# Kernel tuning notes

Measured on AMD Instinct MI355X. Metric: run time of the kernel, lower is better.

## Reference

```python
import jax, jax.numpy as jnp
import numpy as np

N = 50000      # nodes
E = 800000     # edges
F_IN = 128     # num_node_features
H = 128        # hidden_channels
C = 10         # num_classes
G = 512        # graphs in batch


def setup_inputs() -> dict:
    key = jax.random.key(0)
    ks = jax.random.split(key, 8)
    x = jax.random.normal(ks[0], (N, F_IN), dtype=jnp.float32)
    edge_index = jax.random.randint(ks[1], (2, E), 0, N, dtype=jnp.int64)
    batch = jnp.sort(jax.random.randint(ks[2], (N,), 0, G, dtype=jnp.int64))
    s = 1.0 / np.sqrt(F_IN)
    W1 = jax.random.normal(ks[3], (F_IN, H), dtype=jnp.float32) * s
    b1 = jnp.zeros((H,), dtype=jnp.float32)
    W2 = jax.random.normal(ks[4], (H, H), dtype=jnp.float32) * s
    b2 = jnp.zeros((H,), dtype=jnp.float32)
    Wl = jax.random.normal(ks[5], (H, C), dtype=jnp.float32) * s
    bl = jnp.zeros((C,), dtype=jnp.float32)
    return {"x": x, "edge_index": edge_index, "batch": batch,
            "W1": W1, "b1": b1, "W2": W2, "b2": b2, "Wl": Wl, "bl": bl}


def _gcn_conv(h, src, dst, deg_inv_sqrt, W, b):
    # PyG GCNConv: x @ W, then symmetric-normalized scatter-add with self-loops.
    h = h @ W                                   # [N, H]
    norm = deg_inv_sqrt[src] * deg_inv_sqrt[dst]  # [E]
    msg = h[src] * norm[:, None]                # gather + scale, [E, H]
    out = jax.ops.segment_sum(msg, dst, num_segments=N)
    # self-loop contribution (deg already includes +1):
    out = out + h * (deg_inv_sqrt * deg_inv_sqrt)[:, None]
    return out + b


def reference(x, edge_index, batch, W1, b1, W2, b2, Wl, bl):
    src, dst = edge_index[0], edge_index[1]
    # degree on destination nodes, +1 for self-loops (PyG default)
    deg = jax.ops.segment_sum(jnp.ones((E,), x.dtype), dst, num_segments=N) + 1.0
    deg_inv_sqrt = jax.lax.rsqrt(deg)

    h = jax.nn.relu(_gcn_conv(x, src, dst, deg_inv_sqrt, W1, b1))
    h = jax.nn.relu(_gcn_conv(h, src, dst, deg_inv_sqrt, W2, b2))

    # global mean pool over graphs
    sums = jax.ops.segment_sum(h, batch, num_segments=G)          # [G, H]
    counts = jax.ops.segment_sum(jnp.ones((N,), h.dtype), batch, num_segments=G)
    pooled = sums / jnp.clip(counts, 1.0)[:, None]
    # dropout p=0.5 is identity in eval mode
    return pooled @ Wl + bl
```

## Files before the change

### kernel.cpp

```cpp
#include <hip/hip_runtime.h>
#include <hip/hip_bf16.h>
#include <hip/hip_fp16.h>

typedef unsigned short ushort_t;
typedef unsigned int uint32;
typedef __attribute__((ext_vector_type(8))) _Float16 half8;
typedef __attribute__((ext_vector_type(4))) float floatx4;

#define KMAX 64
#define BSHIFT 6
#define BCAP2 1280
#define MAXBUK 800

__device__ __forceinline__ uint32 pack2h(float a, float b) {
    return (uint32)__half_as_ushort(__float2half(a)) |
           ((uint32)__half_as_ushort(__float2half(b)) << 16);
}
__device__ __forceinline__ float2 unpack2h(uint32 q) {
    __half2 hh = *reinterpret_cast<__half2*>(&q);
    return __half22float2(hh);
}

__global__ __launch_bounds__(256) void binmm_k(
    const int* __restrict__ ei, int* __restrict__ bcur,
    uint32* __restrict__ binned, int E, int nbuk, int BB,
    const float* __restrict__ x, const float* __restrict__ W,
    uint32* __restrict__ t2, int N,
    const int* __restrict__ batch, int* __restrict__ gstart, int G) {
    __shared__ __align__(16) char smem[34816];
    int tid = threadIdx.x;
    if (blockIdx.x < BB) {
        int* hist = (int*)smem;
        int* lbase = hist + MAXBUK;
        for (int i = tid; i < nbuk; i += 256) hist[i] = 0;
        __syncthreads();
        int base = blockIdx.x * 4096;
        uint32 ed[16];
        int bk[16];
        #pragma unroll
        for (int i = 0; i < 16; ++i) {
            int e = base + i * 256 + tid;
            if (e < E) {
                int s = ei[e], d = ei[E + e];
                ed[i] = (uint32)s | ((uint32)d << 16);
                bk[i] = d >> BSHIFT;
                atomicAdd(&hist[bk[i]], 1);
            } else bk[i] = -1;
        }
        __syncthreads();
        for (int i = tid; i < nbuk; i += 256) lbase[i] = atomicAdd(&bcur[i], hist[i]);
        __syncthreads();
        for (int i = tid; i < nbuk; i += 256) hist[i] = 0;
        __syncthreads();
        #pragma unroll
        for (int i = 0; i < 16; ++i) {
            if (bk[i] >= 0) {
                int p = atomicAdd(&hist[bk[i]], 1);
                int idx = lbase[bk[i]] + p;
                if (idx < BCAP2) binned[(size_t)bk[i] * BCAP2 + idx] = ed[i];
            }
        }
    } else {
        int bid = blockIdx.x - BB;
        int i0 = bid * 256 + tid;
        if (i0 <= G) {
            int lo = 0, hi = N;
            while (lo < hi) {
                int mid = (lo + hi) >> 1;
                if (batch[mid] < i0) lo = mid + 1; else hi = mid;
            }
            gstart[i0] = lo;
        }
        ushort_t (*Wh)[136] = (ushort_t(*)[136])smem;
        for (int i = tid; i < 128 * 128; i += 256) {
            int k = i >> 7, c = i & 127;
            Wh[c][k] = __half_as_ushort(__float2half(W[i]));
        }
        __syncthreads();

        int wave = tid >> 6, lane = tid & 63;
        int row0 = bid * 64 + wave * 16;
        int m = lane & 15;
        int arow = row0 + m;
        int koff = (lane >> 4) * 8;
        bool valid = arow < N;

        floatx4 acc[8];
        #pragma unroll
        for (int nt = 0; nt < 8; ++nt) acc[nt] = (floatx4){0.f, 0.f, 0.f, 0.f};

        for (int kk = 0; kk < 4; ++kk) {
            int k = kk * 32 + koff;
            union { uint32 u[4]; half8 h; } av;
            av.u[0] = av.u[1] = av.u[2] = av.u[3] = 0;
            if (valid) {
                const float* p = x + (size_t)arow * 128 + k;
                floatx4 f0 = *(const floatx4*)p;
                floatx4 f1 = *(const floatx4*)(p + 4);
                av.u[0] = pack2h(f0[0], f0[1]);
                av.u[1] = pack2h(f0[2], f0[3]);
                av.u[2] = pack2h(f1[0], f1[1]);
                av.u[3] = pack2h(f1[2], f1[3]);
            }
            half8 af = av.h;
            #pragma unroll
            for (int nt = 0; nt < 8; ++nt) {
                int col = nt * 16 + m;
                half8 bf = *(const half8*)(&Wh[col][k]);
                acc[nt] = __builtin_amdgcn_mfma_f32_16x16x32_f16(af, bf, acc[nt], 0, 0, 0);
            }
        }
        int r0 = (lane >> 4) * 4;
        #pragma unroll
        for (int nt = 0; nt < 4; ++nt) {
            int c = nt * 16 + m;
            #pragma unroll
            for (int r = 0; r < 4; ++r) {
                int row = row0 + r0 + r;
                if (row < N)
                    t2[(size_t)row * 64 + c] = pack2h(acc[nt][r], acc[nt + 4][r]);
            }
        }
    }
}

__global__ __launch_bounds__(256) void fill4_k(const uint32* __restrict__ binned,
                                               const int* __restrict__ bcur,
                                               int* __restrict__ cnt,
                                               ushort_t* __restrict__ slot,
                                               uint32* __restrict__ t2, int N) {
    __shared__ uint32 ls[64 * KMAX / 2];
    __shared__ int lc[64];
    __shared__ float dsf[64];
    int b = blockIdx.x;
    int tid = threadIdx.x;
    if (tid < 64) lc[tid] = 0;
    uint32 sv2 = (uint32)(ushort_t)N | ((uint32)(ushort_t)N << 16);
    for (int i = tid; i < 64 * KMAX / 2; i += 256) ls[i] = sv2;
    __syncthreads();
    int ne = bcur[b];
    if (ne > BCAP2) ne = BCAP2;
    const uint32* src = binned + (size_t)b * BCAP2;
    int nbase = b << BSHIFT;
    ushort_t* lsu = (ushort_t*)ls;
    for (int i = tid; i < ne; i += 256) {
        uint32 ed = src[i];
        int s = (int)(ed & 0xFFFFu);
        int d = (int)(ed >> 16) - nbase;
        int p = atomicAdd(&lc[d], 1);
        if (p < KMAX) lsu[(d << 6) + p] = (ushort_t)s;
    }
    __syncthreads();
    int nn = N - nbase;
    if (nn > 64) nn = 64;
    if (tid < 64) {
        if (tid < nn) cnt[nbase + tid] = lc[tid];
        dsf[tid] = rsqrtf((float)lc[tid] + 1.0f);
    }
    uint4* gs = (uint4*)(slot + ((size_t)nbase << 6));
    const uint4* lsv = (const uint4*)ls;
    int totalv = nn * 8;
    for (int i = tid; i < totalv; i += 256) gs[i] = lsv[i];
    __syncthreads();
    int tot = nn * 64;
    for (int i = tid; i < tot; i += 256) {
        int r = i >> 6, c = i & 63;
        size_t idx = ((size_t)(nbase + r) << 6) + c;
        float ds = dsf[r];
        float2 f = unpack2h(t2[idx]);
        t2[idx] = pack2h(f.x * ds, f.y * ds);
    }
}

__device__ __forceinline__ void gather16(const uint32* __restrict__ t2,
                                         const ushort_t* __restrict__ sl,
                                         int lane, float& acc0, float& acc1) {
    uint4 qa = *(const uint4*)(sl);
    uint4 qb = *(const uint4*)(sl + 8);
    uint32 sw[8] = {qa.x, qa.y, qa.z, qa.w, qb.x, qb.y, qb.z, qb.w};
    int s[16];
    #pragma unroll
    for (int u = 0; u < 8; ++u) {
        s[2 * u] = (int)(sw[u] & 0xFFFFu);
        s[2 * u + 1] = (int)(sw[u] >> 16);
    }
    float2 f[16];
    #pragma unroll
    for (int u = 0; u < 16; ++u)
        f[u] = unpack2h(t2[(size_t)s[u] * 64 + lane]);
    #pragma unroll
    for (int u = 0; u < 16; ++u) {
        acc0 += f[u].x;
        acc1 += f[u].y;
    }
}

__global__ __launch_bounds__(256) void agg_k(const uint32* __restrict__ t2,
                                             const int* __restrict__ cnt,
                                             const ushort_t* __restrict__ slot,
                                             const float* __restrict__ bias,
                                             uint32* __restrict__ outp, int N) {
    int wave = threadIdx.x >> 6, lane = threadIdx.x & 63;
    int n = blockIdx.x * 4 + wave;
    if (n >= N) return;
    int deg = cnt[n];
    float d = rsqrtf((float)deg + 1.0f);
    if (deg > KMAX) deg = KMAX;
    float2 self = unpack2h(t2[(size_t)n * 64 + lane]);
    float acc0 = self.x;
    float acc1 = self.y;
    const ushort_t* sl = slot + (size_t)n * KMAX;
    int rounds = (deg + 15) >> 4;
    for (int rr = 0; rr < rounds; ++rr)
        gather16(t2, sl + rr * 16, lane, acc0, acc1);
    acc0 = fmaxf(acc0 * d + bias[lane], 0.f);
    acc1 = fmaxf(acc1 * d + bias[lane + 64], 0.f);
    outp[(size_t)n * 64 + lane] = pack2h(acc0, acc1);
}

__global__ __launch_bounds__(256) void gemm2_k(const uint32* __restrict__ Av,
                                               const float* __restrict__ W,
                                               uint32* __restrict__ t2, int N,
                                               const int* __restrict__ cnt) {
    int tid = threadIdx.x;
    __shared__ ushort_t Wh[128][136];
    for (int i = tid; i < 128 * 128; i += 256) {
        int k = i >> 7, c = i & 127;
        Wh[c][k] = __half_as_ushort(__float2half(W[i]));
    }
    __syncthreads();

    int wave = tid >> 6, lane = tid & 63;
    int row0 = blockIdx.x * 64 + wave * 16;
    int m = lane & 15;
    int arow = row0 + m;
    int koff = (lane >> 4) * 8;
    bool valid = arow < N;

    floatx4 acc[8];
    #pragma unroll
    for (int nt = 0; nt < 8; ++nt) acc[nt] = (floatx4){0.f, 0.f, 0.f, 0.f};

    for (int kk = 0; kk < 4; ++kk) {
        int k = kk * 32 + koff;
        union { uint32 u[4]; half8 h; } av;
        av.u[0] = av.u[1] = av.u[2] = av.u[3] = 0;
        if (valid) {
            const uint32* hp = Av + (size_t)arow * 64 + (k & 63);
            uint4 w0 = *(const uint4*)hp;
            uint4 w1 = *(const uint4*)(hp + 4);
            uint32 ws[8] = {w0.x, w0.y, w0.z, w0.w, w1.x, w1.y, w1.z, w1.w};
            if (k >= 64) {
                #pragma unroll
                for (int j = 0; j < 4; ++j)
                    av.u[j] = (ws[2 * j] >> 16) | (ws[2 * j + 1] & 0xFFFF0000u);
            } else {
                #pragma unroll
                for (int j = 0; j < 4; ++j)
                    av.u[j] = (ws[2 * j] & 0xFFFFu) | (ws[2 * j + 1] << 16);
            }
        }
        half8 af = av.h;
        #pragma unroll
        for (int nt = 0; nt < 8; ++nt) {
            int col = nt * 16 + m;
            half8 bf = *(const half8*)(&Wh[col][k]);
            acc[nt] = __builtin_amdgcn_mfma_f32_16x16x32_f16(af, bf, acc[nt], 0, 0, 0);
        }
    }

    int r0 = (lane >> 4) * 4;
    float dsc[4];
    #pragma unroll
    for (int r = 0; r < 4; ++r) {
        int row = row0 + r0 + r;
        dsc[r] = (row < N) ? rsqrtf((float)cnt[row] + 1.0f) : 0.f;
    }
    #pragma unroll
    for (int nt = 0; nt < 4; ++nt) {
        int c = nt * 16 + m;
        #pragma unroll
        for (int r = 0; r < 4; ++r) {
            int row = row0 + r0 + r;
            if (row < N)
                t2[(size_t)row * 64 + c] =
                    pack2h(acc[nt][r] * dsc[r], acc[nt + 4][r] * dsc[r]);
        }
    }
}

__global__ __launch_bounds__(256) void aggpool_k(const uint32* __restrict__ t2,
                                                 const int* __restrict__ cnt,
                                                 const ushort_t* __restrict__ slot,
                                                 const float* __restrict__ bias,
                                                 const int* __restrict__ batch,
                                                 float* __restrict__ gsum, int N) {
    int wave = threadIdx.x >> 6, lane = threadIdx.x & 63;
    int n = blockIdx.x * 4 + wave;
    if (n >= N) return;
    int deg = cnt[n];
    float d = rsqrtf((float)deg + 1.0f);
    if (deg > KMAX) deg = KMAX;
    float2 self = unpack2h(t2[(size_t)n * 64 + lane]);
    float acc0 = self.x;
    float acc1 = self.y;
    const ushort_t* sl = slot + (size_t)n * KMAX;
    int rounds = (deg + 15) >> 4;
    for (int rr = 0; rr < rounds; ++rr)
        gather16(t2, sl + rr * 16, lane, acc0, acc1);
    acc0 = fmaxf(acc0 * d + bias[lane], 0.f);
    acc1 = fmaxf(acc1 * d + bias[lane + 64], 0.f);
    int g = batch[n];
    atomicAdd(&gsum[(size_t)g * 128 + lane], acc0);
    atomicAdd(&gsum[(size_t)g * 128 + 64 + lane], acc1);
}

__global__ __launch_bounds__(128) void poolfin_k(const float* __restrict__ gsum,
                                                 const int* __restrict__ gstart,
                                                 const float* __restrict__ Wl,
                                                 const float* __restrict__ bl,
                                                 float* __restrict__ out, int C) {
    __shared__ float m[128];
    int g = blockIdx.x;
    float inv = 1.f / fmaxf((float)(gstart[g + 1] - gstart[g]), 1.f);
    m[threadIdx.x] = gsum[(size_t)g * 128 + threadIdx.x] * inv;
    __syncthreads();
    if (threadIdx.x < C) {
        float sum = bl[threadIdx.x];
        #pragma unroll 4
        for (int jj = 0; jj < 128; ++jj)
            sum += m[jj] * Wl[jj * C + threadIdx.x];
        out[g * C + threadIdx.x] = sum;
    }
}

extern "C" void kernel_launch(void* const* d_in, const int* in_sizes, int n_in,
                              void* d_out, int out_size, void* d_ws, size_t ws_size,
                              hipStream_t stream) {
    const float* x   = (const float*)d_in[0];
    const int* ei    = (const int*)d_in[1];
    const int* batch = (const int*)d_in[2];
    const float* W1  = (const float*)d_in[3];
    const float* b1  = (const float*)d_in[4];
    const float* W2  = (const float*)d_in[5];
    const float* b2  = (const float*)d_in[6];
    const float* Wl  = (const float*)d_in[7];
    const float* bl  = (const float*)d_in[8];
    float* out = (float*)d_out;

    int N = in_sizes[2];
    int E = in_sizes[1] / 2;
    int C = in_sizes[8];
    int G = out_size / C;
    int nbuk = (N + 63) >> BSHIFT;

    char* w = (char*)d_ws;
    auto alloc = [&](size_t bytes) -> void* {
        void* p = (void*)w;
        w += (bytes + 255) & ~(size_t)255;
        return p;
    };
    int* bcur       = (int*)alloc((size_t)nbuk * 4);
    int* cnt        = (int*)alloc((size_t)N * 4);
    int* gstart     = (int*)alloc((size_t)(G + 1) * 4);
    ushort_t* slot  = (ushort_t*)alloc((size_t)nbuk * 64 * KMAX * 2);
    uint32* binned  = (uint32*)alloc((size_t)nbuk * BCAP2 * 4);
    uint32* t2      = (uint32*)alloc((size_t)(N + 1) * 64 * 4);
    uint32* h1      = (uint32*)alloc((size_t)N * 64 * 4);
    uint32* t2b     = (uint32*)alloc((size_t)(N + 1) * 64 * 4);
    float* gsum     = (float*)alloc((size_t)G * 128 * 4);

    hipMemsetAsync(bcur, 0, (size_t)nbuk * 4, stream);
    hipMemsetAsync(gsum, 0, (size_t)G * 128 * 4, stream);
    hipMemsetAsync(t2 + (size_t)N * 64, 0, 256, stream);
    hipMemsetAsync(t2b + (size_t)N * 64, 0, 256, stream);

    int GB = (N + 63) / 64;
    int AB = (N + 3) / 4;
    int BB = (E + 4095) / 4096;

    binmm_k<<<BB + GB, 256, 0, stream>>>(ei, bcur, binned, E, nbuk, BB,
                                         x, W1, t2, N, batch, gstart, G);
    fill4_k<<<nbuk, 256, 0, stream>>>(binned, bcur, cnt, slot, t2, N);
    agg_k<<<AB, 256, 0, stream>>>(t2, cnt, slot, b1, h1, N);
    gemm2_k<<<GB, 256, 0, stream>>>(h1, W2, t2b, N, cnt);
    aggpool_k<<<AB, 256, 0, stream>>>(t2b, cnt, slot, b2, batch, gsum, N);
    poolfin_k<<<G, 128, 0, stream>>>(gsum, gstart, Wl, bl, out, C);
}
```

Baseline: 202.0 us.

## Replace bucketed edge binning with direct global-atomic slot fill and drop fill kernel

Removes the two-phase bucket sort (shared histogram plus binned buffer) and the fill4_k kernel. Edges are now placed straight into per-node slot lists with global atomics on cnt, and the padding is a 0xFF sentinel set by a memset. Source-side degree scaling moves into the aggregation gather, which reads cnt for each neighbour and applies rsqrt there. Memsets for gsum and the sentinel rows are folded into the first kernel. In exchange there are heavily contended random global atomics, an extra memset of the slot array (about 6.4 MB), and an extra cnt load plus rsqrt per gathered neighbour. gemm2_k and aggpool_k are not shown changing, so if the scaling is not moved there too, layer-2 results may be wrong.

```diff
diff --git a/kernel.cpp b/kernel.cpp
--- a/kernel.cpp
+++ b/kernel.cpp
@@ -8,9 +8,7 @@
 typedef __attribute__((ext_vector_type(4))) float floatx4;
 
 #define KMAX 64
-#define BSHIFT 6
-#define BCAP2 1280
-#define MAXBUK 800
+#define SENT 65535
 
 __device__ __forceinline__ uint32 pack2h(float a, float b) {
     return (uint32)__half_as_ushort(__float2half(a)) |
@@ -22,43 +20,28 @@
 }
 
 __global__ __launch_bounds__(256) void binmm_k(
-    const int* __restrict__ ei, int* __restrict__ bcur,
-    uint32* __restrict__ binned, int E, int nbuk, int BB,
+    const int* __restrict__ ei, int* __restrict__ cnt,
+    ushort_t* __restrict__ slot, int E, int BB,
     const float* __restrict__ x, const float* __restrict__ W,
-    uint32* __restrict__ t2, int N,
+    uint32* __restrict__ t2, uint32* __restrict__ t2b,
+    float* __restrict__ gsum, int GS, int N,
     const int* __restrict__ batch, int* __restrict__ gstart, int G) {
-    __shared__ __align__(16) char smem[34816];
     int tid = threadIdx.x;
     if (blockIdx.x < BB) {
-        int* hist = (int*)smem;
-        int* lbase = hist + MAXBUK;
-        for (int i = tid; i < nbuk; i += 256) hist[i] = 0;
-        __syncthreads();
         int base = blockIdx.x * 4096;
-        uint32 ed[16];
-        int bk[16];
         #pragma unroll
         for (int i = 0; i < 16; ++i) {
             int e = base + i * 256 + tid;
             if (e < E) {
                 int s = ei[e], d = ei[E + e];
-                ed[i] = (uint32)s | ((uint32)d << 16);
-                bk[i] = d >> BSHIFT;
-                atomicAdd(&hist[bk[i]], 1);
-            } else bk[i] = -1;
-        }
-        __syncthreads();
-        for (int i = tid; i < nbuk; i += 256) lbase[i] = atomicAdd(&bcur[i], hist[i]);
-        __syncthreads();
-        for (int i = tid; i < nbuk; i += 256) hist[i] = 0;
-        __syncthreads();
-        #pragma unroll
-        for (int i = 0; i < 16; ++i) {
-            if (bk[i] >= 0) {
-                int p = atomicAdd(&hist[bk[i]], 1);
-                int idx = lbase[bk[i]] + p;
-                if (idx < BCAP2) binned[(size_t)bk[i] * BCAP2 + idx] = ed[i];
-            }
+                int p = atomicAdd(&cnt[d], 1);
+                if (p < KMAX) slot[(size_t)d * KMAX + p] = (ushort_t)s;
+            }
+        }
+        for (int i = blockIdx.x * 256 + tid; i < GS; i += BB * 256) gsum[i] = 0.f;
+        if (blockIdx.x == 0 && tid < 64) {
+            t2[(size_t)SENT * 64 + tid] = 0u;
+            t2b[(size_t)SENT * 64 + tid] = 0u;
         }
     } else {
         int bid = blockIdx.x - BB;
@@ -71,7 +54,7 @@
             }
             gstart[i0] = lo;
         }
-        ushort_t (*Wh)[136] = (ushort_t(*)[136])smem;
+        __shared__ ushort_t Wh[128][136];
         for (int i = tid; i < 128 * 128; i += 256) {
             int k = i >> 7, c = i & 127;
             Wh[c][k] = __half_as_ushort(__float2half(W[i]));
@@ -124,51 +107,30 @@
     }
 }
 
-__global__ __launch_bounds__(256) void fill4_k(const uint32* __restrict__ binned,
-                                               const int* __restrict__ bcur,
-                                               int* __restrict__ cnt,
-                                               ushort_t* __restrict__ slot,
-                                               uint32* __restrict__ t2, int N) {
-    __shared__ uint32 ls[64 * KMAX / 2];
-    __shared__ int lc[64];
-    __shared__ float dsf[64];
-    int b = blockIdx.x;
-    int tid = threadIdx.x;
-    if (tid < 64) lc[tid] = 0;
-    uint32 sv2 = (uint32)(ushort_t)N | ((uint32)(ushort_t)N << 16);
-    for (int i = tid; i < 64 * KMAX / 2; i += 256) ls[i] = sv2;
-    __syncthreads();
-    int ne = bcur[b];
-    if (ne > BCAP2) ne = BCAP2;
-    const uint32* src = binned + (size_t)b * BCAP2;
-    int nbase = b << BSHIFT;
-    ushort_t* lsu = (ushort_t*)ls;
-    for (int i = tid; i < ne; i += 256) {
-        uint32 ed = src[i];
-        int s = (int)(ed & 0xFFFFu);
-        int d = (int)(ed >> 16) - nbase;
-        int p = atomicAdd(&lc[d], 1);
-        if (p < KMAX) lsu[(d << 6) + p] = (ushort_t)s;
-    }
-    __syncthreads();
-    int nn = N - nbase;
-    if (nn > 64) nn = 64;
-    if (tid < 64) {
-        if (tid < nn) cnt[nbase + tid] = lc[tid];
-        dsf[tid] = rsqrtf((float)lc[tid] + 1.0f);
-    }
-    uint4* gs = (uint4*)(slot + ((size_t)nbase << 6));
-    const uint4* lsv = (const uint4*)ls;
-    int totalv = nn * 8;
-    for (int i = tid; i < totalv; i += 256) gs[i] = lsv[i];
-    __syncthreads();
-    int tot = nn * 64;
-    for (int i = tid; i < tot; i += 256) {
-        int r = i >> 6, c = i & 63;
-        size_t idx = ((size_t)(nbase + r) << 6) + c;
-        float ds = dsf[r];
-        float2 f = unpack2h(t2[idx]);
-        t2[idx] = pack2h(f.x * ds, f.y * ds);
+__device__ __forceinline__ void gather16s(const uint32* __restrict__ t2,
+                                          const int* __restrict__ cnt,
+                                          const ushort_t* __restrict__ sl,
+                                          int lane, float& acc0, float& acc1) {
+    uint4 qa = *(const uint4*)(sl);
+    uint4 qb = *(const uint4*)(sl + 8);
+    uint32 sw[8] = {qa.x, qa.y, qa.z, qa.w, qb.x, qb.y, qb.z, qb.w};
+    int s[16];
+    #pragma unroll
+    for (int u = 0; u < 8; ++u) {
+        s[2 * u] = (int)(sw[u] & 0xFFFFu);
+        s[2 * u + 1] = (int)(sw[u] >> 16);
+    }
+    float2 f[16];
+    float ds[16];
+    #pragma unroll
+    for (int u = 0; u < 16; ++u) {
+        f[u] = unpack2h(t2[(size_t)s[u] * 64 + lane]);
+        ds[u] = rsqrtf((float)cnt[s[u]] + 1.0f);
+    }
+    #pragma unroll
+    for (int u = 0; u < 16; ++u) {
+        acc0 = fmaf(f[u].x, ds[u], acc0);
+        acc1 = fmaf(f[u].y, ds[u], acc1);
     }
 }
 
@@ -207,12 +169,12 @@
     float d = rsqrtf((float)deg + 1.0f);
     if (deg > KMAX) deg = KMAX;
     float2 self = unpack2h(t2[(size_t)n * 64 + lane]);
-    float acc0 = self.x;
-    float acc1 = self.y;
+    float acc0 = self.x * d;
+    float acc1 = self.y * d;
     const ushort_t* sl = slot + (size_t)n * KMAX;
     int rounds = (deg + 15) >> 4;
     for (int rr = 0; rr < rounds; ++rr)
-        gather16(t2, sl + rr * 16, lane, acc0, acc1);
+        gather16s(t2, cnt, sl + rr * 16, lane, acc0, acc1);
     acc0 = fmaxf(acc0 * d + bias[lane], 0.f);
     acc1 = fmaxf(acc1 * d + bias[lane + 64], 0.f);
     outp[(size_t)n * 64 + lane] = pack2h(acc0, acc1);
@@ -352,7 +314,6 @@
     int E = in_sizes[1] / 2;
     int C = in_sizes[8];
     int G = out_size / C;
-    int nbuk = (N + 63) >> BSHIFT;
 
     char* w = (char*)d_ws;
     auto alloc = [&](size_t bytes) -> void* {
@@ -360,28 +321,24 @@
         w += (bytes + 255) & ~(size_t)255;
         return p;
     };
-    int* bcur       = (int*)alloc((size_t)nbuk * 4);
-    int* cnt        = (int*)alloc((size_t)N * 4);
+    int* cnt        = (int*)alloc((size_t)65536 * 4);
     int* gstart     = (int*)alloc((size_t)(G + 1) * 4);
-    ushort_t* slot  = (ushort_t*)alloc((size_t)nbuk * 64 * KMAX * 2);
-    uint32* binned  = (uint32*)alloc((size_t)nbuk * BCAP2 * 4);
-    uint32* t2      = (uint32*)alloc((size_t)(N + 1) * 64 * 4);
+    ushort_t* slot  = (ushort_t*)alloc((size_t)N * KMAX * 2);
+    uint32* t2      = (uint32*)alloc((size_t)65536 * 64 * 4);
     uint32* h1      = (uint32*)alloc((size_t)N * 64 * 4);
-    uint32* t2b     = (uint32*)alloc((size_t)(N + 1) * 64 * 4);
+    uint32* t2b     = (uint32*)alloc((size_t)65536 * 64 * 4);
     float* gsum     = (float*)alloc((size_t)G * 128 * 4);
 
-    hipMemsetAsync(bcur, 0, (size_t)nbuk * 4, stream);
-    hipMemsetAsync(gsum, 0, (size_t)G * 128 * 4, stream);
-    hipMemsetAsync(t2 + (size_t)N * 64, 0, 256, stream);
-    hipMemsetAsync(t2b + (size_t)N * 64, 0, 256, stream);
+    hipMemsetAsync(cnt, 0, (size_t)65536 * 4, stream);
+    hipMemsetAsync(slot, 0xFF, (size_t)N * KMAX * 2, stream);
 
     int GB = (N + 63) / 64;
     int AB = (N + 3) / 4;
     int BB = (E + 4095) / 4096;
 
-    binmm_k<<<BB + GB, 256, 0, stream>>>(ei, bcur, binned, E, nbuk, BB,
-                                         x, W1, t2, N, batch, gstart, G);
-    fill4_k<<<nbuk, 256, 0, stream>>>(binned, bcur, cnt, slot, t2, N);
+    binmm_k<<<BB + GB, 256, 0, stream>>>(ei, cnt, slot, E, BB,
+                                         x, W1, t2, t2b, gsum, G * 128, N,
+                                         batch, gstart, G);
     agg_k<<<AB, 256, 0, stream>>>(t2, cnt, slot, b1, h1, N);
     gemm2_k<<<GB, 256, 0, stream>>>(h1, W2, t2b, N, cnt);
     aggpool_k<<<AB, 256, 0, stream>>>(t2b, cnt, slot, b2, batch, gsum, N);
```

Result: slower. 219.7 us (+8.8%).

## Move source-degree scaling into layer-1 gather and fold memsets into binning kernel

Applied to the files above, without the earlier changes.

The pass in fill4_k that rescaled t2 by each node's deg^-1/2 is removed. The layer-1 aggregation now reads cnt for every gathered neighbour and applies the rsqrt scale on the fly, with the self term scaled by d. The separate memsets for gsum and the t2/t2b padding rows are folded into the binning blocks of binmm_k, and cnt gets a padding entry at index N for the sentinel slot. This removes a read-modify-write over t2 and three memset launches, but adds an extra scattered cnt load and an rsqrt for each edge in agg_k.

```diff
diff --git a/kernel.cpp b/kernel.cpp
--- a/kernel.cpp
+++ b/kernel.cpp
@@ -25,7 +25,8 @@
     const int* __restrict__ ei, int* __restrict__ bcur,
     uint32* __restrict__ binned, int E, int nbuk, int BB,
     const float* __restrict__ x, const float* __restrict__ W,
-    uint32* __restrict__ t2, int N,
+    uint32* __restrict__ t2, uint32* __restrict__ t2b,
+    float* __restrict__ gsum, int GS, int* __restrict__ cnt, int N,
     const int* __restrict__ batch, int* __restrict__ gstart, int G) {
     __shared__ __align__(16) char smem[34816];
     int tid = threadIdx.x;
@@ -59,6 +60,14 @@
                 int idx = lbase[bk[i]] + p;
                 if (idx < BCAP2) binned[(size_t)bk[i] * BCAP2 + idx] = ed[i];
             }
+        }
+        for (int i = blockIdx.x * 256 + tid; i < GS; i += BB * 256) gsum[i] = 0.f;
+        if (blockIdx.x == 0) {
+            if (tid < 64) {
+                t2[(size_t)N * 64 + tid] = 0u;
+                t2b[(size_t)N * 64 + tid] = 0u;
+            }
+            if (tid == 0) cnt[N] = 0;
         }
     } else {
         int bid = blockIdx.x - BB;
@@ -127,11 +136,9 @@
 __global__ __launch_bounds__(256) void fill4_k(const uint32* __restrict__ binned,
                                                const int* __restrict__ bcur,
                                                int* __restrict__ cnt,
-                                               ushort_t* __restrict__ slot,
-                                               uint32* __restrict__ t2, int N) {
+                                               ushort_t* __restrict__ slot, int N) {
     __shared__ uint32 ls[64 * KMAX / 2];
     __shared__ int lc[64];
-    __shared__ float dsf[64];
     int b = blockIdx.x;
     int tid = threadIdx.x;
     if (tid < 64) lc[tid] = 0;
@@ -153,22 +160,37 @@
     __syncthreads();
     int nn = N - nbase;
     if (nn > 64) nn = 64;
-    if (tid < 64) {
-        if (tid < nn) cnt[nbase + tid] = lc[tid];
-        dsf[tid] = rsqrtf((float)lc[tid] + 1.0f);
-    }
+    if (tid < 64 && tid < nn) cnt[nbase + tid] = lc[tid];
     uint4* gs = (uint4*)(slot + ((size_t)nbase << 6));
     const uint4* lsv = (const uint4*)ls;
     int totalv = nn * 8;
     for (int i = tid; i < totalv; i += 256) gs[i] = lsv[i];
-    __syncthreads();
-    int tot = nn * 64;
-    for (int i = tid; i < tot; i += 256) {
-        int r = i >> 6, c = i & 63;
-        size_t idx = ((size_t)(nbase + r) << 6) + c;
-        float ds = dsf[r];
-        float2 f = unpack2h(t2[idx]);
-        t2[idx] = pack2h(f.x * ds, f.y * ds);
+}
+
+__device__ __forceinline__ void gather16s(const uint32* __restrict__ t2,
+                                          const int* __restrict__ cnt,
+                                          const ushort_t* __restrict__ sl,
+                                          int lane, float& acc0, float& acc1) {
+    uint4 qa = *(const uint4*)(sl);
+    uint4 qb = *(const uint4*)(sl + 8);
+    uint32 sw[8] = {qa.x, qa.y, qa.z, qa.w, qb.x, qb.y, qb.z, qb.w};
+    int s[16];
+    #pragma unroll
+    for (int u = 0; u < 8; ++u) {
+        s[2 * u] = (int)(sw[u] & 0xFFFFu);
+        s[2 * u + 1] = (int)(sw[u] >> 16);
+    }
+    float2 f[16];
+    float ds[16];
+    #pragma unroll
+    for (int u = 0; u < 16; ++u) {
+        f[u] = unpack2h(t2[(size_t)s[u] * 64 + lane]);
+        ds[u] = rsqrtf((float)cnt[s[u]] + 1.0f);
+    }
+    #pragma unroll
+    for (int u = 0; u < 16; ++u) {
+        acc0 = fmaf(f[u].x, ds[u], acc0);
+        acc1 = fmaf(f[u].y, ds[u], acc1);
     }
 }
 
@@ -207,12 +229,12 @@
     float d = rsqrtf((float)deg + 1.0f);
     if (deg > KMAX) deg = KMAX;
     float2 self = unpack2h(t2[(size_t)n * 64 + lane]);
-    float acc0 = self.x;
-    float acc1 = self.y;
+    float acc0 = self.x * d;
+    float acc1 = self.y * d;
     const ushort_t* sl = slot + (size_t)n * KMAX;
     int rounds = (deg + 15) >> 4;
     for (int rr = 0; rr < rounds; ++rr)
-        gather16(t2, sl + rr * 16, lane, acc0, acc1);
+        gather16s(t2, cnt, sl + rr * 16, lane, acc0, acc1);
     acc0 = fmaxf(acc0 * d + bias[lane], 0.f);
     acc1 = fmaxf(acc1 * d + bias[lane + 64], 0.f);
     outp[(size_t)n * 64 + lane] = pack2h(acc0, acc1);
@@ -361,7 +383,7 @@
         return p;
     };
     int* bcur       = (int*)alloc((size_t)nbuk * 4);
-    int* cnt        = (int*)alloc((size_t)N * 4);
+    int* cnt        = (int*)alloc((size_t)(N + 1) * 4);
     int* gstart     = (int*)alloc((size_t)(G + 1) * 4);
     ushort_t* slot  = (ushort_t*)alloc((size_t)nbuk * 64 * KMAX * 2);
     uint32* binned  = (uint32*)alloc((size_t)nbuk * BCAP2 * 4);
@@ -371,17 +393,15 @@
     float* gsum     = (float*)alloc((size_t)G * 128 * 4);
 
     hipMemsetAsync(bcur, 0, (size_t)nbuk * 4, stream);
-    hipMemsetAsync(gsum, 0, (size_t)G * 128 * 4, stream);
-    hipMemsetAsync(t2 + (size_t)N * 64, 0, 256, stream);
-    hipMemsetAsync(t2b + (size_t)N * 64, 0, 256, stream);
 
     int GB = (N + 63) / 64;
     int AB = (N + 3) / 4;
     int BB = (E + 4095) / 4096;
 
     binmm_k<<<BB + GB, 256, 0, stream>>>(ei, bcur, binned, E, nbuk, BB,
-                                         x, W1, t2, N, batch, gstart, G);
-    fill4_k<<<nbuk, 256, 0, stream>>>(binned, bcur, cnt, slot, t2, N);
+                                         x, W1, t2, t2b, gsum, G * 128, cnt, N,
+                                         batch, gstart, G);
+    fill4_k<<<nbuk, 256, 0, stream>>>(binned, bcur, cnt, slot, N);
     agg_k<<<AB, 256, 0, stream>>>(t2, cnt, slot, b1, h1, N);
     gemm2_k<<<GB, 256, 0, stream>>>(h1, W2, t2b, N, cnt);
     aggpool_k<<<AB, 256, 0, stream>>>(t2b, cnt, slot, b2, batch, gsum, N);
```

Result: no change. 203.7 us (+0.9%).
